# Optimization experiments

Measured on AMD Instinct MI355X. Metric: run time of the kernel, lower is better.

The kernel has to match this reference:

```python
import jax, jax.numpy as jnp
import numpy as np

NEG_POS_RATIO = 3  # neg_pos_ratio from __init__
B, P, C = 64, 8732, 81  # batch, num_priors(SSD300), num_classes (COCO+bg)


def hard_negative_mining(loss, labels, neg_pos_ratio):
    # loss: (B,P) background -log_softmax; labels: (B,P) int
    pos_mask = labels > 0
    num_pos = pos_mask.sum(axis=1, keepdims=True)
    num_neg = num_pos * neg_pos_ratio
    loss = jnp.where(pos_mask, -jnp.inf, loss)  # exclude positives from mining
    indexes = jnp.argsort(-loss, axis=1)        # descending sort of losses
    orders = jnp.argsort(indexes, axis=1)       # rank of each prior
    neg_mask = orders < num_neg                 # top num_neg hardest negatives
    return pos_mask | neg_mask


def setup_inputs() -> dict:
    key = jax.random.key(0)
    k1, k2, k3, k4, k5 = jax.random.split(key, 5)
    confidence = jax.random.normal(k1, (B, P, C), dtype=jnp.float32)
    predicted_locations = jax.random.normal(k2, (B, P, 4), dtype=jnp.float32)
    raw_labels = jax.random.randint(k3, (B, P), 1, C)
    is_pos = jax.random.uniform(k4, (B, P)) < 0.05
    labels = jnp.where(is_pos, raw_labels, 0).astype(jnp.int64)
    gt_locations = jax.random.normal(k5, (B, P, 4), dtype=jnp.float32)
    return {"confidence": confidence, "predicted_locations": predicted_locations,
            "labels": labels, "gt_locations": gt_locations}


def reference(confidence, predicted_locations, labels, gt_locations):
    # ---- hard negative mining (no_grad in the original) ----
    bg_loss = -jax.nn.log_softmax(jax.lax.stop_gradient(confidence), axis=2)[:, :, 0]
    mask = hard_negative_mining(bg_loss, labels, NEG_POS_RATIO)  # (B,P) bool

    # ---- masked cross-entropy (reduction='sum' over selected priors) ----
    logp = jax.nn.log_softmax(confidence, axis=2)                 # (B,P,C)
    ce = -jnp.take_along_axis(logp, labels[..., None], axis=2)[..., 0]  # (B,P)
    classification_loss = jnp.sum(jnp.where(mask, ce, 0.0))

    # ---- smooth L1 over positive priors (reduction='sum', beta=1) ----
    pos_mask = labels > 0
    diff = jnp.abs(predicted_locations - gt_locations)
    sl1 = jnp.where(diff < 1.0, 0.5 * diff * diff, diff - 0.5)    # (B,P,4)
    smooth_l1_loss = jnp.sum(jnp.where(pos_mask[..., None], sl1, 0.0))

    num_pos = jnp.sum(pos_mask).astype(confidence.dtype)          # gt_locations.size(0)
    return smooth_l1_loss / num_pos, classification_loss / num_pos
```

## Files before the change

### kernel.cpp

```cpp
#include <hip/hip_runtime.h>
#include <math.h>

#define NB 64
#define NP 8732
#define NC 81
#define NROWS (NB * NP)
#define TPB 256
#define NBLK (NROWS / TPB)
#define SEL_TPB 1024
#define SKPT 9
#define STAIL (NP - 8 * SEL_TPB)

#define PART_OFF 64
#define PART_BYTES (((NBLK * 3 * 8 + 63) / 64) * 64)
#define KEY_OFF (PART_OFF + PART_BYTES)

__global__ __launch_bounds__(TPB) void mb_rows(
    const float* __restrict__ conf,
    const float* __restrict__ pred,
    const float* __restrict__ gt,
    const int*   __restrict__ labels,
    unsigned* __restrict__ keys,
    double* __restrict__ partials,
    double* __restrict__ acc)
{
    __shared__ double s_red[4][3];

    const int tid = threadIdx.x;
    const int row = blockIdx.x * TPB + tid;

    if (blockIdx.x == 0 && tid == 0) {
        acc[0] = 0.0; acc[1] = 0.0; acc[2] = 0.0; acc[3] = 0.0; acc[4] = 0.0;
    }

    const float* rp = conf + (size_t)row * NC;

    float4 q[20];
    #pragma unroll
    for (int i = 0; i < 20; ++i) __builtin_memcpy(&q[i], rp + 4 * i, 16);
    const float last = rp[80];

    float4 m4 = q[0];
    #pragma unroll
    for (int i = 1; i < 20; ++i) {
        m4.x = fmaxf(m4.x, q[i].x);
        m4.y = fmaxf(m4.y, q[i].y);
        m4.z = fmaxf(m4.z, q[i].z);
        m4.w = fmaxf(m4.w, q[i].w);
    }
    float M = fmaxf(fmaxf(m4.x, m4.y), fmaxf(m4.z, m4.w));
    M = fmaxf(M, last);

    float s = __expf(last - M);
    #pragma unroll
    for (int i = 0; i < 20; ++i)
        s += __expf(q[i].x - M) + __expf(q[i].y - M)
           + __expf(q[i].z - M) + __expf(q[i].w - M);

    const float lse = M + __logf(s);

    double ce = 0.0, sl = 0.0, npd = 0.0;
    const int lbl = labels[row];
    unsigned key = 0u;
    if (lbl > 0) {
        ce  = (double)(lse - rp[lbl]);
        npd = 1.0;
        const float4 pv = ((const float4*)pred)[row];
        const float4 gv = ((const float4*)gt)[row];
        float d;
        d = fabsf(pv.x - gv.x); sl += (d < 1.f) ? 0.5f * d * d : d - 0.5f;
        d = fabsf(pv.y - gv.y); sl += (d < 1.f) ? 0.5f * d * d : d - 0.5f;
        d = fabsf(pv.z - gv.z); sl += (d < 1.f) ? 0.5f * d * d : d - 0.5f;
        d = fabsf(pv.w - gv.w); sl += (d < 1.f) ? 0.5f * d * d : d - 0.5f;
    } else {
        key = __float_as_uint(lse - q[0].x) + 1u;
    }
    keys[row] = key;

    #pragma unroll
    for (int o = 32; o; o >>= 1) {
        ce  += __shfl_xor(ce, o);
        sl  += __shfl_xor(sl, o);
        npd += __shfl_xor(npd, o);
    }
    const int wid = tid >> 6, lane = tid & 63;
    if (lane == 0) { s_red[wid][0] = ce; s_red[wid][1] = sl; s_red[wid][2] = npd; }
    __syncthreads();
    if (tid == 0) {
        double a = 0, b = 0, c = 0;
        for (int w = 0; w < 4; ++w) { a += s_red[w][0]; b += s_red[w][1]; c += s_red[w][2]; }
        partials[blockIdx.x * 3 + 0] = a;
        partials[blockIdx.x * 3 + 1] = b;
        partials[blockIdx.x * 3 + 2] = c;
    }
}

__global__ __launch_bounds__(SEL_TPB) void mb_select(
    const unsigned* __restrict__ keys_g,
    const double* __restrict__ partials,
    double* __restrict__ acc,
    float* __restrict__ out)
{
    __shared__ unsigned cnt[34];
    __shared__ unsigned s_np[16], s_mx[16], s_mn[16], s_cg[16];
    __shared__ double   s_sum[16];
    __shared__ double   s_pp[3];
    __shared__ unsigned s_K, s_lo, s_hi;

    const int b = blockIdx.x, tid = threadIdx.x;
    const int lane = tid & 63, wid = tid >> 6;

    if (wid == 0) {
        double pce = 0, psl = 0, pnp = 0;
        const int j = b + (lane << 6);
        if (j < NBLK) {
            pce = partials[3 * j + 0];
            psl = partials[3 * j + 1];
            pnp = partials[3 * j + 2];
        }
        #pragma unroll
        for (int o = 32; o; o >>= 1) {
            pce += __shfl_xor(pce, o);
            psl += __shfl_xor(psl, o);
            pnp += __shfl_xor(pnp, o);
        }
        if (lane == 0) { s_pp[0] = pce; s_pp[1] = psl; s_pp[2] = pnp; }
    }

    unsigned k[SKPT];
    unsigned np = 0, mx = 0u, mn = 0xFFFFFFFFu;
    #pragma unroll
    for (int i = 0; i < SKPT; ++i) {
        unsigned key = 0u;
        if (i < 8 || tid < STAIL) {
            key = keys_g[b * NP + i * SEL_TPB + tid];
            np += (key == 0u) ? 1u : 0u;
            if (key) { mx = max(mx, key); mn = min(mn, key); }
        }
        k[i] = key;
    }
    if (tid < 34) cnt[tid] = 0u;

    #pragma unroll
    for (int o = 32; o; o >>= 1) {
        np += __shfl_xor(np, o);
        mx  = max(mx, __shfl_xor(mx, o));
        mn  = min(mn, __shfl_xor(mn, o));
    }
    if (lane == 0) { s_np[wid] = np; s_mx[wid] = mx; s_mn[wid] = mn; }
    __syncthreads();

    if (tid == 0) {
        unsigned npt = 0, MX = 0, MN = 0xFFFFFFFFu;
        for (int q = 0; q < 16; ++q) {
            npt += s_np[q];
            MX = max(MX, s_mx[q]); MN = min(MN, s_mn[q]);
        }
        atomicAdd(&acc[1], s_pp[0]);
        atomicAdd(&acc[2], s_pp[1]);
        atomicAdd(&acc[3], s_pp[2]);
        unsigned K = 3u * npt;
        const unsigned nneg = NP - npt;
        if (K > nneg) K = nneg;
        s_K = K; s_lo = MN; s_hi = MX;
    }
    __syncthreads();

    const unsigned K = s_K;
    if (K > 0) {
        unsigned lo = s_lo, hi = s_hi;
        int it = 0;
        while (lo < hi) {
            const unsigned mid = lo + ((hi - lo) >> 1);
            unsigned c = 0;
            #pragma unroll
            for (int i = 0; i < SKPT; ++i) c += (k[i] > mid) ? 1u : 0u;
            #pragma unroll
            for (int o = 32; o; o >>= 1) c += __shfl_xor(c, o);
            if (lane == 0) atomicAdd(&cnt[it], c);
            __syncthreads();
            if (cnt[it] < K) hi = mid; else lo = mid + 1;
            ++it;
        }
        const unsigned V = lo;

        double ssum = 0.0; unsigned cgt = 0;
        #pragma unroll
        for (int i = 0; i < SKPT; ++i) {
            const unsigned kk = k[i];
            if (kk > V) { ssum += (double)__uint_as_float(kk - 1u); cgt++; }
        }
        #pragma unroll
        for (int o = 32; o; o >>= 1) { ssum += __shfl_xor(ssum, o); cgt += __shfl_xor(cgt, o); }
        if (lane == 0) { s_sum[wid] = ssum; s_cg[wid] = cgt; }
        __syncthreads();
        if (tid == 0) {
            double tot = 0.0; unsigned cg = 0;
            for (int q = 0; q < 16; ++q) { tot += s_sum[q]; cg += s_cg[q]; }
            tot += (double)(K - cg) * (double)__uint_as_float(V - 1u);
            atomicAdd(&acc[0], tot);
        }
    }

    if (tid == 0) {
        __threadfence();
        const unsigned done = atomicAdd((unsigned*)(acc + 4), 1u);
        if (done == NB - 1) {
            __threadfence();
            const double topk = atomicAdd(&acc[0], 0.0);
            const double pce  = atomicAdd(&acc[1], 0.0);
            const double psl  = atomicAdd(&acc[2], 0.0);
            const double npd  = atomicAdd(&acc[3], 0.0);
            out[0] = (float)(psl / npd);
            out[1] = (float)((pce + topk) / npd);
        }
    }
}

extern "C" void kernel_launch(void* const* d_in, const int* in_sizes, int n_in,
                              void* d_out, int out_size, void* d_ws, size_t ws_size,
                              hipStream_t stream)
{
    const float* conf   = (const float*)d_in[0];
    const float* pred   = (const float*)d_in[1];
    const int*   labels = (const int*)d_in[2];
    const float* gt     = (const float*)d_in[3];
    float* out = (float*)d_out;

    double*   acc      = (double*)d_ws;
    double*   partials = (double*)((char*)d_ws + PART_OFF);
    unsigned* keys     = (unsigned*)((char*)d_ws + KEY_OFF);

    mb_rows<<<NBLK, TPB, 0, stream>>>(conf, pred, gt, labels, keys, partials, acc);
    mb_select<<<NB, SEL_TPB, 0, stream>>>(keys, partials, acc, out);
}
```

Before: 56.74 us.

## Use 4-way radix search with fewer block barriers in top-k selection

The threshold search in the selection kernel now tests three pivots per iteration, splitting the range into quarters. This halves the number of block-wide barrier and shared-atomic rounds, at the cost of three counts per round instead of one. The block size is also halved to 512 threads with 18 keys per thread, which means fewer warps per barrier and more register-held keys. An iteration cap of 20 is added as a safety bound.

```diff
diff --git a/kernel.cpp b/kernel.cpp
--- a/kernel.cpp
+++ b/kernel.cpp
@@ -7,9 +7,9 @@
 #define NROWS (NB * NP)
 #define TPB 256
 #define NBLK (NROWS / TPB)
-#define SEL_TPB 1024
-#define SKPT 9
-#define STAIL (NP - 8 * SEL_TPB)
+#define SEL_TPB 512
+#define SKPT 18
+#define STAIL (NP - 17 * SEL_TPB)
 
 #define PART_OFF 64
 #define PART_BYTES (((NBLK * 3 * 8 + 63) / 64) * 64)
@@ -101,9 +101,9 @@
     double* __restrict__ acc,
     float* __restrict__ out)
 {
-    __shared__ unsigned cnt[34];
-    __shared__ unsigned s_np[16], s_mx[16], s_mn[16], s_cg[16];
-    __shared__ double   s_sum[16];
+    __shared__ unsigned cnt[3][20];
+    __shared__ unsigned s_np[8], s_mx[8], s_mn[8], s_cg[8];
+    __shared__ double   s_sum[8];
     __shared__ double   s_pp[3];
     __shared__ unsigned s_K, s_lo, s_hi;
 
@@ -132,14 +132,14 @@
     #pragma unroll
     for (int i = 0; i < SKPT; ++i) {
         unsigned key = 0u;
-        if (i < 8 || tid < STAIL) {
+        if (i < 17 || tid < STAIL) {
             key = keys_g[b * NP + i * SEL_TPB + tid];
             np += (key == 0u) ? 1u : 0u;
             if (key) { mx = max(mx, key); mn = min(mn, key); }
         }
         k[i] = key;
     }
-    if (tid < 34) cnt[tid] = 0u;
+    if (tid < 60) ((unsigned*)cnt)[tid] = 0u;
 
     #pragma unroll
     for (int o = 32; o; o >>= 1) {
@@ -152,7 +152,7 @@
 
     if (tid == 0) {
         unsigned npt = 0, MX = 0, MN = 0xFFFFFFFFu;
-        for (int q = 0; q < 16; ++q) {
+        for (int q = 0; q < 8; ++q) {
             npt += s_np[q];
             MX = max(MX, s_mx[q]); MN = min(MN, s_mn[q]);
         }
@@ -170,16 +170,36 @@
     if (K > 0) {
         unsigned lo = s_lo, hi = s_hi;
         int it = 0;
-        while (lo < hi) {
-            const unsigned mid = lo + ((hi - lo) >> 1);
-            unsigned c = 0;
+        while (lo < hi && it < 20) {
+            const unsigned span = hi - lo;
+            const unsigned m1 = lo + (span >> 2);
+            const unsigned m2 = lo + (span >> 1);
+            const unsigned m3 = lo + span - (span >> 2);
+            unsigned c1 = 0, c2 = 0, c3 = 0;
             #pragma unroll
-            for (int i = 0; i < SKPT; ++i) c += (k[i] > mid) ? 1u : 0u;
+            for (int i = 0; i < SKPT; ++i) {
+                const unsigned kk = k[i];
+                c1 += (kk > m1) ? 1u : 0u;
+                c2 += (kk > m2) ? 1u : 0u;
+                c3 += (kk > m3) ? 1u : 0u;
+            }
             #pragma unroll
-            for (int o = 32; o; o >>= 1) c += __shfl_xor(c, o);
-            if (lane == 0) atomicAdd(&cnt[it], c);
+            for (int o = 32; o; o >>= 1) {
+                c1 += __shfl_xor(c1, o);
+                c2 += __shfl_xor(c2, o);
+                c3 += __shfl_xor(c3, o);
+            }
+            if (lane == 0) {
+                atomicAdd(&cnt[0][it], c1);
+                atomicAdd(&cnt[1][it], c2);
+                atomicAdd(&cnt[2][it], c3);
+            }
             __syncthreads();
-            if (cnt[it] < K) hi = mid; else lo = mid + 1;
+            const unsigned n1 = cnt[0][it], n2 = cnt[1][it], n3 = cnt[2][it];
+            if (n1 < K)      { hi = m1; }
+            else if (n2 < K) { lo = m1 + 1; hi = m2; }
+            else if (n3 < K) { lo = m2 + 1; hi = m3; }
+            else             { lo = m3 + 1; }
             ++it;
         }
         const unsigned V = lo;
@@ -196,7 +216,7 @@
         __syncthreads();
         if (tid == 0) {
             double tot = 0.0; unsigned cg = 0;
-            for (int q = 0; q < 16; ++q) { tot += s_sum[q]; cg += s_cg[q]; }
+            for (int q = 0; q < 8; ++q) { tot += s_sum[q]; cg += s_cg[q]; }
             tot += (double)(K - cg) * (double)__uint_as_float(V - 1u);
             atomicAdd(&acc[0], tot);
         }
```

Measured after the change: 57.89 us. 1.02x slower.

## Fuse row pass and per-batch top-k selection into one kernel via completion counters

Applied to the files above, without the earlier changes.

Merges the row-wise logsumexp kernel and the per-batch hard-negative selection kernel into a single launch. Each block atomically adds its finished-row count to a per-batch counter, and the block that completes a batch runs the threshold search for it with 256 threads holding 35 keys each. Per-block partial sums now go straight to global atomics instead of a partials buffer, and a memset zeroes the counters. This removes the second launch and the serialization between the two kernels, but the selection now runs with 256 threads instead of 1024 per batch, under register pressure from 35 keys per thread, and the last blocks to finish must each run a full selection.

```diff
diff --git a/kernel.cpp b/kernel.cpp
--- a/kernel.cpp
+++ b/kernel.cpp
@@ -7,31 +7,32 @@
 #define NROWS (NB * NP)
 #define TPB 256
 #define NBLK (NROWS / TPB)
-#define SEL_TPB 1024
-#define SKPT 9
-#define STAIL (NP - 8 * SEL_TPB)
-
-#define PART_OFF 64
-#define PART_BYTES (((NBLK * 3 * 8 + 63) / 64) * 64)
-#define KEY_OFF (PART_OFF + PART_BYTES)
-
-__global__ __launch_bounds__(TPB) void mb_rows(
+#define KPT 35
+#define KTAIL (NP - 34 * 256)
+
+#define DONE_OFF 64
+#define KEY_OFF  384
+
+__global__ __launch_bounds__(TPB) void mb_all(
     const float* __restrict__ conf,
     const float* __restrict__ pred,
     const float* __restrict__ gt,
     const int*   __restrict__ labels,
     unsigned* __restrict__ keys,
-    double* __restrict__ partials,
-    double* __restrict__ acc)
+    unsigned* __restrict__ done,
+    double* __restrict__ acc,
+    float* __restrict__ out)
 {
     __shared__ double s_red[4][3];
+    __shared__ int s_mine[2];
+    __shared__ unsigned cnt[34];
+    __shared__ unsigned s_np[4], s_mx[4], s_mn[4], s_cg[4];
+    __shared__ double   s_sum[4];
+    __shared__ unsigned s_K, s_lo, s_hi;
 
     const int tid = threadIdx.x;
     const int row = blockIdx.x * TPB + tid;
-
-    if (blockIdx.x == 0 && tid == 0) {
-        acc[0] = 0.0; acc[1] = 0.0; acc[2] = 0.0; acc[3] = 0.0; acc[4] = 0.0;
-    }
+    const int lane = tid & 63, wid = tid >> 6;
 
     const float* rp = conf + (size_t)row * NC;
 
@@ -83,137 +84,121 @@
         sl  += __shfl_xor(sl, o);
         npd += __shfl_xor(npd, o);
     }
-    const int wid = tid >> 6, lane = tid & 63;
     if (lane == 0) { s_red[wid][0] = ce; s_red[wid][1] = sl; s_red[wid][2] = npd; }
     __syncthreads();
     if (tid == 0) {
         double a = 0, b = 0, c = 0;
         for (int w = 0; w < 4; ++w) { a += s_red[w][0]; b += s_red[w][1]; c += s_red[w][2]; }
-        partials[blockIdx.x * 3 + 0] = a;
-        partials[blockIdx.x * 3 + 1] = b;
-        partials[blockIdx.x * 3 + 2] = c;
-    }
-}
-
-__global__ __launch_bounds__(SEL_TPB) void mb_select(
-    const unsigned* __restrict__ keys_g,
-    const double* __restrict__ partials,
-    double* __restrict__ acc,
-    float* __restrict__ out)
-{
-    __shared__ unsigned cnt[34];
-    __shared__ unsigned s_np[16], s_mx[16], s_mn[16], s_cg[16];
-    __shared__ double   s_sum[16];
-    __shared__ double   s_pp[3];
-    __shared__ unsigned s_K, s_lo, s_hi;
-
-    const int b = blockIdx.x, tid = threadIdx.x;
-    const int lane = tid & 63, wid = tid >> 6;
-
-    if (wid == 0) {
-        double pce = 0, psl = 0, pnp = 0;
-        const int j = b + (lane << 6);
-        if (j < NBLK) {
-            pce = partials[3 * j + 0];
-            psl = partials[3 * j + 1];
-            pnp = partials[3 * j + 2];
-        }
+        if (a != 0.0) atomicAdd(&acc[1], a);
+        if (b != 0.0) atomicAdd(&acc[2], b);
+        if (c != 0.0) atomicAdd(&acc[3], c);
+
+        const int r0 = blockIdx.x * TPB;
+        const int b0 = r0 / NP;
+        const int end0 = (b0 + 1) * NP;
+        const int contrib0 = (end0 - r0 < TPB) ? (end0 - r0) : TPB;
+        __threadfence();
+        const unsigned o0 = atomicAdd(&done[b0], (unsigned)contrib0);
+        s_mine[0] = (o0 + (unsigned)contrib0 == NP) ? b0 : -1;
+        s_mine[1] = -1;
+        if (contrib0 < TPB) {
+            const int b1 = b0 + 1;
+            const unsigned c1 = (unsigned)(TPB - contrib0);
+            const unsigned o1 = atomicAdd(&done[b1], c1);
+            if (o1 + c1 == NP) s_mine[1] = b1;
+        }
+    }
+    __syncthreads();
+
+    for (int mi = 0; mi < 2; ++mi) {
+        const int b = s_mine[mi];
+        if (b < 0) continue;
+        __threadfence();
+
+        unsigned k[KPT];
+        unsigned np = 0, mx = 0u, mn = 0xFFFFFFFFu;
+        #pragma unroll
+        for (int i = 0; i < KPT; ++i) {
+            unsigned kv = 0u;
+            if (i < 34 || tid < KTAIL) {
+                kv = __hip_atomic_load(&keys[b * NP + i * 256 + tid],
+                                       __ATOMIC_RELAXED, __HIP_MEMORY_SCOPE_AGENT);
+                np += (kv == 0u) ? 1u : 0u;
+                if (kv) { mx = max(mx, kv); mn = min(mn, kv); }
+            }
+            k[i] = kv;
+        }
+        for (int i = tid; i < 34; i += TPB) cnt[i] = 0u;
+
         #pragma unroll
         for (int o = 32; o; o >>= 1) {
-            pce += __shfl_xor(pce, o);
-            psl += __shfl_xor(psl, o);
-            pnp += __shfl_xor(pnp, o);
-        }
-        if (lane == 0) { s_pp[0] = pce; s_pp[1] = psl; s_pp[2] = pnp; }
-    }
-
-    unsigned k[SKPT];
-    unsigned np = 0, mx = 0u, mn = 0xFFFFFFFFu;
-    #pragma unroll
-    for (int i = 0; i < SKPT; ++i) {
-        unsigned key = 0u;
-        if (i < 8 || tid < STAIL) {
-            key = keys_g[b * NP + i * SEL_TPB + tid];
-            np += (key == 0u) ? 1u : 0u;
-            if (key) { mx = max(mx, key); mn = min(mn, key); }
-        }
-        k[i] = key;
-    }
-    if (tid < 34) cnt[tid] = 0u;
-
-    #pragma unroll
-    for (int o = 32; o; o >>= 1) {
-        np += __shfl_xor(np, o);
-        mx  = max(mx, __shfl_xor(mx, o));
-        mn  = min(mn, __shfl_xor(mn, o));
-    }
-    if (lane == 0) { s_np[wid] = np; s_mx[wid] = mx; s_mn[wid] = mn; }
-    __syncthreads();
-
-    if (tid == 0) {
-        unsigned npt = 0, MX = 0, MN = 0xFFFFFFFFu;
-        for (int q = 0; q < 16; ++q) {
-            npt += s_np[q];
-            MX = max(MX, s_mx[q]); MN = min(MN, s_mn[q]);
-        }
-        atomicAdd(&acc[1], s_pp[0]);
-        atomicAdd(&acc[2], s_pp[1]);
-        atomicAdd(&acc[3], s_pp[2]);
-        unsigned K = 3u * npt;
-        const unsigned nneg = NP - npt;
-        if (K > nneg) K = nneg;
-        s_K = K; s_lo = MN; s_hi = MX;
-    }
-    __syncthreads();
-
-    const unsigned K = s_K;
-    if (K > 0) {
-        unsigned lo = s_lo, hi = s_hi;
-        int it = 0;
-        while (lo < hi) {
-            const unsigned mid = lo + ((hi - lo) >> 1);
-            unsigned c = 0;
-            #pragma unroll
-            for (int i = 0; i < SKPT; ++i) c += (k[i] > mid) ? 1u : 0u;
-            #pragma unroll
-            for (int o = 32; o; o >>= 1) c += __shfl_xor(c, o);
-            if (lane == 0) atomicAdd(&cnt[it], c);
-            __syncthreads();
-            if (cnt[it] < K) hi = mid; else lo = mid + 1;
-            ++it;
-        }
-        const unsigned V = lo;
-
-        double ssum = 0.0; unsigned cgt = 0;
-        #pragma unroll
-        for (int i = 0; i < SKPT; ++i) {
-            const unsigned kk = k[i];
-            if (kk > V) { ssum += (double)__uint_as_float(kk - 1u); cgt++; }
-        }
-        #pragma unroll
-        for (int o = 32; o; o >>= 1) { ssum += __shfl_xor(ssum, o); cgt += __shfl_xor(cgt, o); }
-        if (lane == 0) { s_sum[wid] = ssum; s_cg[wid] = cgt; }
+            np += __shfl_xor(np, o);
+            mx  = max(mx, __shfl_xor(mx, o));
+            mn  = min(mn, __shfl_xor(mn, o));
+        }
+        if (lane == 0) { s_np[wid] = np; s_mx[wid] = mx; s_mn[wid] = mn; }
         __syncthreads();
         if (tid == 0) {
-            double tot = 0.0; unsigned cg = 0;
-            for (int q = 0; q < 16; ++q) { tot += s_sum[q]; cg += s_cg[q]; }
-            tot += (double)(K - cg) * (double)__uint_as_float(V - 1u);
-            atomicAdd(&acc[0], tot);
-        }
-    }
-
-    if (tid == 0) {
-        __threadfence();
-        const unsigned done = atomicAdd((unsigned*)(acc + 4), 1u);
-        if (done == NB - 1) {
+            const unsigned npt = s_np[0] + s_np[1] + s_np[2] + s_np[3];
+            unsigned MX = max(max(s_mx[0], s_mx[1]), max(s_mx[2], s_mx[3]));
+            unsigned MN = min(min(s_mn[0], s_mn[1]), min(s_mn[2], s_mn[3]));
+            unsigned K = 3u * npt;
+            const unsigned nneg = NP - npt;
+            if (K > nneg) K = nneg;
+            s_K = K; s_lo = MN; s_hi = MX;
+        }
+        __syncthreads();
+
+        const unsigned K = s_K;
+        if (K > 0) {
+            unsigned lo = s_lo, hi = s_hi;
+            int it = 0;
+            while (lo < hi) {
+                const unsigned mid = lo + ((hi - lo) >> 1);
+                unsigned c = 0;
+                #pragma unroll
+                for (int i = 0; i < KPT; ++i) c += (k[i] > mid) ? 1u : 0u;
+                #pragma unroll
+                for (int o = 32; o; o >>= 1) c += __shfl_xor(c, o);
+                if (lane == 0) atomicAdd(&cnt[it], c);
+                __syncthreads();
+                if (cnt[it] < K) hi = mid; else lo = mid + 1;
+                ++it;
+            }
+            const unsigned V = lo;
+
+            double ssum = 0.0; unsigned cgt = 0;
+            #pragma unroll
+            for (int i = 0; i < KPT; ++i) {
+                const unsigned kk = k[i];
+                if (kk > V) { ssum += (double)__uint_as_float(kk - 1u); cgt++; }
+            }
+            #pragma unroll
+            for (int o = 32; o; o >>= 1) { ssum += __shfl_xor(ssum, o); cgt += __shfl_xor(cgt, o); }
+            if (lane == 0) { s_sum[wid] = ssum; s_cg[wid] = cgt; }
+            __syncthreads();
+            if (tid == 0) {
+                double tot = s_sum[0] + s_sum[1] + s_sum[2] + s_sum[3];
+                const unsigned cg = s_cg[0] + s_cg[1] + s_cg[2] + s_cg[3];
+                tot += (double)(K - cg) * (double)__uint_as_float(V - 1u);
+                atomicAdd(&acc[0], tot);
+            }
+        }
+
+        if (tid == 0) {
             __threadfence();
-            const double topk = atomicAdd(&acc[0], 0.0);
-            const double pce  = atomicAdd(&acc[1], 0.0);
-            const double psl  = atomicAdd(&acc[2], 0.0);
-            const double npd  = atomicAdd(&acc[3], 0.0);
-            out[0] = (float)(psl / npd);
-            out[1] = (float)((pce + topk) / npd);
-        }
+            const unsigned t = atomicAdd((unsigned*)(acc + 4), 1u);
+            if (t == NB - 1) {
+                __threadfence();
+                const double topk = atomicAdd(&acc[0], 0.0);
+                const double pce  = atomicAdd(&acc[1], 0.0);
+                const double psl  = atomicAdd(&acc[2], 0.0);
+                const double npt  = atomicAdd(&acc[3], 0.0);
+                out[0] = (float)(psl / npt);
+                out[1] = (float)((pce + topk) / npt);
+            }
+        }
+        __syncthreads();
     }
 }
 
@@ -227,10 +212,10 @@
     const float* gt     = (const float*)d_in[3];
     float* out = (float*)d_out;
 
-    double*   acc      = (double*)d_ws;
-    double*   partials = (double*)((char*)d_ws + PART_OFF);
-    unsigned* keys     = (unsigned*)((char*)d_ws + KEY_OFF);
-
-    mb_rows<<<NBLK, TPB, 0, stream>>>(conf, pred, gt, labels, keys, partials, acc);
-    mb_select<<<NB, SEL_TPB, 0, stream>>>(keys, partials, acc, out);
+    double*   acc  = (double*)d_ws;
+    unsigned* done = (unsigned*)((char*)d_ws + DONE_OFF);
+    unsigned* keys = (unsigned*)((char*)d_ws + KEY_OFF);
+
+    hipMemsetAsync(d_ws, 0, KEY_OFF, stream);
+    mb_all<<<NBLK, TPB, 0, stream>>>(conf, pred, gt, labels, keys, done, acc, out);
 }
```

Result: slower. 205.1 us (+261.6%).

## Replace binary-search threshold selection with multi-pass radix-256 histogram select

Applied to the files above, without the earlier changes.

The per-batch top-K threshold search no longer bisects over 32-bit keys, which took about 32 rounds, each with a block-wide count and a barrier. It now runs a radix-style select: each pass builds per-wave shared-memory histograms over 256 bins, sums them, and uses a wave-level suffix scan to find the bin holding the K-th largest key, which narrows the range roughly 256x per pass. The goal is fewer block-wide synchronisation rounds. In exchange each pass adds shared-memory atomics, histogram clearing and extra barriers, and the block uses more shared memory.

```diff
diff --git a/kernel.cpp b/kernel.cpp
--- a/kernel.cpp
+++ b/kernel.cpp
@@ -10,6 +10,8 @@
 #define SEL_TPB 1024
 #define SKPT 9
 #define STAIL (NP - 8 * SEL_TPB)
+#define NWAVE 16
+#define HPAD 257
 
 #define PART_OFF 64
 #define PART_BYTES (((NBLK * 3 * 8 + 63) / 64) * 64)
@@ -101,11 +103,12 @@
     double* __restrict__ acc,
     float* __restrict__ out)
 {
-    __shared__ unsigned cnt[34];
+    __shared__ unsigned whist[NWAVE][HPAD];
+    __shared__ unsigned tot[256];
     __shared__ unsigned s_np[16], s_mx[16], s_mn[16], s_cg[16];
     __shared__ double   s_sum[16];
     __shared__ double   s_pp[3];
-    __shared__ unsigned s_K, s_lo, s_hi;
+    __shared__ unsigned s_K, s_lo, s_hi, s_bin, s_newA;
 
     const int b = blockIdx.x, tid = threadIdx.x;
     const int lane = tid & 63, wid = tid >> 6;
@@ -139,7 +142,6 @@
         }
         k[i] = key;
     }
-    if (tid < 34) cnt[tid] = 0u;
 
     #pragma unroll
     for (int o = 32; o; o >>= 1) {
@@ -168,19 +170,63 @@
 
     const unsigned K = s_K;
     if (K > 0) {
-        unsigned lo = s_lo, hi = s_hi;
-        int it = 0;
-        while (lo < hi) {
-            const unsigned mid = lo + ((hi - lo) >> 1);
-            unsigned c = 0;
+        unsigned lo = s_lo, hi = s_hi, A = 0u;
+        for (int pass = 0; pass < 5 && lo < hi; ++pass) {
+            const unsigned span  = hi - lo;
+            const unsigned width = span / 256u + 1u;
+
+            for (int i = tid; i < NWAVE * HPAD; i += SEL_TPB)
+                ((unsigned*)whist)[i] = 0u;
+            __syncthreads();
+
             #pragma unroll
-            for (int i = 0; i < SKPT; ++i) c += (k[i] > mid) ? 1u : 0u;
-            #pragma unroll
-            for (int o = 32; o; o >>= 1) c += __shfl_xor(c, o);
-            if (lane == 0) atomicAdd(&cnt[it], c);
-            __syncthreads();
-            if (cnt[it] < K) hi = mid; else lo = mid + 1;
-            ++it;
+            for (int i = 0; i < SKPT; ++i) {
+                const unsigned kk = k[i];
+                if (kk >= lo && kk <= hi)
+                    atomicAdd(&whist[wid][(kk - lo) / width], 1u);
+            }
+            __syncthreads();
+
+            if (tid < 256) {
+                unsigned t = 0;
+                #pragma unroll
+                for (int w = 0; w < NWAVE; ++w) t += whist[w][tid];
+                tot[tid] = t;
+            }
+            __syncthreads();
+
+            if (tid < 64) {
+                const int l = tid;
+                const unsigned c0 = tot[4 * l], c1 = tot[4 * l + 1];
+                const unsigned c2 = tot[4 * l + 2], c3 = tot[4 * l + 3];
+                const unsigned ls = c0 + c1 + c2 + c3;
+                unsigned run = ls;
+                #pragma unroll
+                for (int off = 1; off < 64; off <<= 1) {
+                    const unsigned o = __shfl_down(run, off);
+                    if (l + off < 64) run += o;
+                }
+                unsigned above = A + (run - ls);
+                const unsigned cs[4] = {c3, c2, c1, c0};
+                #pragma unroll
+                for (int q = 0; q < 4; ++q) {
+                    const unsigned c = cs[q];
+                    if (above < K && above + c >= K) {
+                        s_bin  = (unsigned)(4 * l + 3 - q);
+                        s_newA = above;
+                    }
+                    above += c;
+                }
+            }
+            __syncthreads();
+
+            const unsigned j = s_bin;
+            A = s_newA;
+            const unsigned nlo = lo + j * width;
+            unsigned nhi = nlo + width - 1u;
+            if (nhi > hi) nhi = hi;
+            lo = nlo; hi = nhi;
+            __syncthreads();
         }
         const unsigned V = lo;
 
@@ -195,10 +241,10 @@
         if (lane == 0) { s_sum[wid] = ssum; s_cg[wid] = cgt; }
         __syncthreads();
         if (tid == 0) {
-            double tot = 0.0; unsigned cg = 0;
-            for (int q = 0; q < 16; ++q) { tot += s_sum[q]; cg += s_cg[q]; }
-            tot += (double)(K - cg) * (double)__uint_as_float(V - 1u);
-            atomicAdd(&acc[0], tot);
+            double tot2 = 0.0; unsigned cg = 0;
+            for (int q = 0; q < 16; ++q) { tot2 += s_sum[q]; cg += s_cg[q]; }
+            tot2 += (double)(K - cg) * (double)__uint_as_float(V - 1u);
+            atomicAdd(&acc[0], tot2);
         }
     }
 
```

Measured after the change: 49.61 us. -12.6%, faster.
